# Performance work log

Hardware: AMD Instinct MI355X
Metric: run time of the kernel (lower is better)

Reference implementation:

```python
import jax, jax.numpy as jnp
import numpy as np

N_SERIES = 100000
INPUT_SIZE = 28
OUTPUT_SIZE = 7
N_T = 1
N_S = 4
PERIOD = 7            # seasonality = [7]
EMBED = 1 + 1 + PERIOD  # lev_sms, seas_sms, init seasonal factors
BATCH = 2048
N_TIME = 2048


def setup_inputs() -> dict:
    key = jax.random.key(0)
    k1, k2, k3, k4 = jax.random.split(key, 4)
    # Y must be strictly positive (multiplicative model: division + log)
    Y = jax.random.uniform(k1, (BATCH, N_TIME), dtype=jnp.float32, minval=0.5, maxval=1.5)
    X = jax.random.normal(k2, (BATCH, N_T, N_TIME), dtype=jnp.float32)
    S = jax.random.normal(k3, (BATCH, N_S), dtype=jnp.float32)
    idxs = jax.random.randint(k4, (BATCH,), 0, N_SERIES)
    embeds_weight = jnp.full((N_SERIES, EMBED), 0.5, dtype=jnp.float32)
    return {"S": S, "Y": Y, "X": X, "idxs": idxs,
            "embeds_weight": embeds_weight, "step_size": 7}


def _levels_seasons(Y, idxs, embeds_weight):
    """Exponential smoothing level/seasonality recurrence (single seasonality)."""
    emb = embeds_weight[idxs]                      # (B, 9)
    lev_sms = jax.nn.sigmoid(emb[:, 0])            # (B,)
    seas_sms = jax.nn.sigmoid(emb[:, 1])           # (B,)
    init_seas = jnp.exp(emb[:, 2:2 + PERIOD])      # (B, 7)

    level0 = Y[:, 0] / init_seas[:, 0]
    # ring buffer holding the seasonal factors used at steps t=1..: [s1..s6, s0]
    buf0 = jnp.concatenate([init_seas[:, 1:], init_seas[:, :1]], axis=1)  # (B, 7)

    def step(carry, inp):
        lev, buf = carry
        y, k = inp
        s = jnp.take(buf, k % PERIOD, axis=1)                       # seasonality at lag PERIOD
        newlev = lev_sms * (y / s) + (1.0 - lev_sms) * lev
        news = seas_sms * (y / newlev) + (1.0 - seas_sms) * s
        buf = jax.lax.dynamic_update_slice_in_dim(buf, news[:, None], k % PERIOD, axis=1)
        return (newlev, buf), (newlev, news)

    ks = jnp.arange(N_TIME - 1, dtype=jnp.int32)
    (_, _), (levs, seas) = jax.lax.scan(step, (level0, buf0), (Y[:, 1:].T, ks))
    levels = jnp.concatenate([level0[:, None], levs.T], axis=1)           # (B, n_time)
    seasonal = jnp.concatenate([init_seas, init_seas[:, :1], seas.T], axis=1)  # (B, n_time+7)
    return levels, seasonal


def reference(S, Y, X, idxs, embeds_weight, step_size):
    levels, seasonal = _levels_seasons(Y, idxs, embeds_weight)

    windows_end = N_TIME - INPUT_SIZE - OUTPUT_SIZE + 1
    windows = np.arange(0, windows_end, step_size)          # static window starts
    W = len(windows)

    # --- insample windows, normalized: log(Y / level / season) ---
    idx_in = windows[:, None] + np.arange(INPUT_SIZE)       # (W, I)
    Yw = Y[:, idx_in]                                       # (B, W, I)
    lev_w = levels[:, windows + INPUT_SIZE - 1]             # (B, W)
    seas_w = seasonal[:, idx_in]                            # (B, W, I)
    y_in = jnp.log(Yw / (lev_w[:, :, None] * seas_w))
    y_in = y_in.transpose(1, 0, 2)                          # (W, B, I)

    # --- exogenous windows: X[:, :, start:start+I+O].reshape(B, -1) ---
    idx_x = windows[:, None] + np.arange(INPUT_SIZE + OUTPUT_SIZE)  # (W, I+O)
    Xw = X[:, :, idx_x].transpose(2, 0, 1, 3).reshape(W, BATCH, N_T * (INPUT_SIZE + OUTPUT_SIZE))

    # --- static features ---
    Sw = jnp.broadcast_to(S[None], (W, BATCH, N_S))

    windows_y_insample = jnp.concatenate([y_in, Xw, Sw], axis=2)   # (W, B, context)

    # --- outsample windows (eval mode: not normalized) ---
    idx_out = windows[:, None] + INPUT_SIZE + np.arange(OUTPUT_SIZE)  # (W, O)
    windows_y_outsample = Y[:, idx_out].transpose(1, 0, 2)            # (W, B, O)

    return windows_y_insample, windows_y_outsample, levels, seasonal
```

## Files before the change

### kernel.cpp

```cpp
#include <hip/hip_runtime.h>
#include <math.h>

#define BATCH 2048
#define N_TIME 2048
#define INPUT_SIZE 28
#define OUTPUT_SIZE 7
#define N_S 4
#define PERIOD 7
#define EMBED 9
#define SEAS_LEN (N_TIME + PERIOD)
#define W_COUNT 288
#define WB_COUNT (W_COUNT * BATCH)
#define INS_COLS 67
#define OUT0_SIZE (WB_COUNT * INS_COLS)
#define OUT1_SIZE (WB_COUNT * OUTPUT_SIZE)
#define LEV_SIZE (BATCH * N_TIME)
#define SEAS_SIZE (BATCH * SEAS_LEN)

#define M0_COPY (WB_COUNT * 39)
#define M_COPY  (M0_COPY + OUT1_SIZE)
#define COPY_BLOCKS 480
#define GRID1 (32 + COPY_BLOCKS)
#define N_YIN (WB_COUNT * INPUT_SIZE)
#define CUNROLL 16

struct ScanState {
    float lev, lsms, seas_sms, oma, oms;
    float sbuf[PERIOD];
    float rbuf[PERIOD];
    float yp, sp, rnlp, rnsp;
};

template<bool FIRST, bool LAST, bool PREF>
__device__ __forceinline__ void scan_chunk(
    int base, int l,
    const float* __restrict__ Yb,
    float (&cur)[64], float (&nxt)[64],
    float (*__restrict__ tl)[65], float (*__restrict__ ts)[65],
    ScanState& st)
{
    if (PREF) {
#pragma unroll
        for (int k = 0; k < 64; k += 4)
            *(float4*)&nxt[k] = *(const float4*)(Yb + base + 64 + k);
    }
    tl[l][0] = st.lev;
#pragma unroll
    for (int k = 0; k < 64; ++k) {
        if (!LAST || k < 63) {
            float y  = (k < 63) ? cur[k + 1] : nxt[0];
            float s0 = st.sbuf[k % 7];
            float nl = fmaf(st.oma, st.lev, y * st.rbuf[k % 7]);
            st.lev = nl;
            tl[l][k + 1] = nl;
            if (!FIRST || k > 0) {
                float u  = st.yp * st.rnlp;
                float ns = fmaf(st.oms, st.sp, st.seas_sms * u);
                ts[l][k] = ns;
                st.sbuf[(k + 6) % 7] = ns;
                if (!FIRST || k > 1)
                    st.rbuf[(k + 5) % 7] = st.lsms * st.rnsp;
                st.rnsp = __builtin_amdgcn_rcpf(ns);
            }
            float rnl = __builtin_amdgcn_rcpf(nl);
            st.yp = y; st.sp = s0; st.rnlp = rnl;
        }
    }
    if (LAST) {
        float u  = st.yp * st.rnlp;
        float ns = fmaf(st.oms, st.sp, st.seas_sms * u);
        ts[l][63] = ns;
    } else {
        float t0s = st.sbuf[0], t0r = st.rbuf[0];
#pragma unroll
        for (int q = 0; q < PERIOD - 1; ++q) {
            st.sbuf[q] = st.sbuf[q + 1];
            st.rbuf[q] = st.rbuf[q + 1];
        }
        st.sbuf[PERIOD - 1] = t0s;
        st.rbuf[PERIOD - 1] = t0r;
    }
    asm volatile("s_waitcnt lgkmcnt(0)" ::: "memory");
    __builtin_amdgcn_s_barrier();
}

__device__ __forceinline__ void drain_chunk(
    int base, int jr, int km, int r0,
    const float (*__restrict__ tl)[65], const float (*__restrict__ ts)[65],
    float* __restrict__ levels, float* __restrict__ seasonal)
{
    __builtin_amdgcn_s_barrier();
    asm volatile("" ::: "memory");
#pragma unroll
    for (int j0 = 0; j0 < 64; j0 += 4) {
        int j = j0 + jr;
        float vl[4], vs[4];
#pragma unroll
        for (int i = 0; i < 4; ++i) { vl[i] = tl[j][km + i]; vs[i] = ts[j][km + i]; }
        float4 v4; v4.x = vl[0]; v4.y = vl[1]; v4.z = vl[2]; v4.w = vl[3];
        *(float4*)(levels + (size_t)(r0 + j) * N_TIME + base + km) = v4;
        float* srow = seasonal + (size_t)(r0 + j) * SEAS_LEN + base + 7 + km;
#pragma unroll
        for (int i = 0; i < 4; ++i) srow[i] = vs[i];
    }
    asm volatile("s_waitcnt lgkmcnt(0)" ::: "memory");
}

__device__ __forceinline__ void copy_addr(
    unsigned g,
    const float* __restrict__ Y, const float* __restrict__ X,
    const float* __restrict__ S,
    float* __restrict__ out0, float* __restrict__ out1,
    const float*& src, float*& dst)
{
    if (g < M0_COPY) {
        unsigned wb = g / 39u;
        int jj = (int)(g - wb * 39u);
        int w  = (int)(wb >> 11);
        int b  = (int)(wb & (BATCH - 1));
        src = (jj < 35) ? &X[b * N_TIME + w * 7 + jj]
                        : &S[b * N_S + (jj - 35)];
        dst = &out0[(size_t)wb * 67u + 28u + (unsigned)jj];
    } else {
        unsigned e  = g - M0_COPY;
        unsigned wb = e / 7u;
        int m  = (int)(e - wb * 7u);
        int w  = (int)(wb >> 11);
        int b  = (int)(wb & (BATCH - 1));
        src = &Y[b * N_TIME + w * 7 + INPUT_SIZE + m];
        dst = &out1[e];
    }
}

__global__ __launch_bounds__(128, 1) void es_scan_plus(
    const float* __restrict__ Y, const int* __restrict__ idxs,
    const float* __restrict__ emb, const float* __restrict__ X,
    const float* __restrict__ S,
    float* __restrict__ levels, float* __restrict__ seasonal,
    float* __restrict__ out0, float* __restrict__ out1)
{
    __shared__ float tl[2][64][65];
    __shared__ float ts[2][64][65];
    const int tid = threadIdx.x;
    const int l   = tid & 63;

    if (blockIdx.x >= 32) {
        const unsigned stride = COPY_BLOCKS * 128;
        unsigned g = (blockIdx.x - 32) * 128 + tid;
#pragma unroll 1
        for (; g + (CUNROLL - 1) * stride < M_COPY; g += stride * CUNROLL) {
            const float* src[CUNROLL]; float* dst[CUNROLL]; float v[CUNROLL];
#pragma unroll
            for (int u = 0; u < CUNROLL; ++u)
                copy_addr(g + (unsigned)u * stride, Y, X, S, out0, out1, src[u], dst[u]);
#pragma unroll
            for (int u = 0; u < CUNROLL; ++u) v[u] = *src[u];
#pragma unroll
            for (int u = 0; u < CUNROLL; ++u) *dst[u] = v[u];
        }
#pragma unroll 1
        for (; g < M_COPY; g += stride) {
            const float* src; float* dst;
            copy_addr(g, Y, X, S, out0, out1, src, dst);
            *dst = *src;
        }
        return;
    }

    const int r0 = blockIdx.x * 64;
    if (tid < 64) {
        const int b = r0 + l;
        const float* Yb = Y + (size_t)b * N_TIME;
        const float* e  = emb + (size_t)idxs[b] * EMBED;
        ScanState st;
        st.lsms     = 1.0f / (1.0f + __expf(-e[0]));
        st.seas_sms = 1.0f / (1.0f + __expf(-e[1]));
        st.oma = 1.0f - st.lsms;
        st.oms = 1.0f - st.seas_sms;
        float is[PERIOD];
#pragma unroll
        for (int j = 0; j < PERIOD; ++j) is[j] = __expf(e[2 + j]);
        st.lev = Yb[0] / is[0];

        float* seab = seasonal + (size_t)b * SEAS_LEN;
#pragma unroll
        for (int j = 0; j < PERIOD; ++j) seab[j] = is[j];
        ts[0][l][0] = is[0];
#pragma unroll
        for (int j = 0; j < PERIOD; ++j) st.sbuf[j] = is[(j + 1) % PERIOD];
#pragma unroll
        for (int j = 0; j < PERIOD; ++j)
            st.rbuf[j] = st.lsms * __builtin_amdgcn_rcpf(st.sbuf[j]);
        st.yp = 0.0f; st.sp = 1.0f; st.rnlp = 1.0f; st.rnsp = 1.0f;

        float ya[64], yb2[64];
#pragma unroll
        for (int k = 0; k < 64; k += 4)
            *(float4*)&ya[k] = *(const float4*)(Yb + k);

        scan_chunk<true,  false, true >(0, l, Yb, ya, yb2, tl[0], ts[0], st);
#pragma unroll 1
        for (int cc = 0; cc < 15; ++cc) {
            scan_chunk<false, false, true>(64  + cc * 128, l, Yb, yb2, ya, tl[1], ts[1], st);
            scan_chunk<false, false, true>(128 + cc * 128, l, Yb, ya, yb2, tl[0], ts[0], st);
        }
        scan_chunk<false, true,  false>(1984, l, Yb, yb2, ya, tl[1], ts[1], st);
    } else {
        const int jr = l >> 4;
        const int km = (l & 15) * 4;
#pragma unroll 1
        for (int c = 0; c < 32; ++c)
            drain_chunk(c * 64, jr, km, r0, tl[c & 1], ts[c & 1], levels, seasonal);
    }
}

__global__ __launch_bounds__(256) void es_windows_yin(
    const float* __restrict__ Y, const float* __restrict__ levels,
    const float* __restrict__ seasonal, float* __restrict__ out0)
{
    unsigned gid = blockIdx.x * 256 + threadIdx.x;
    unsigned wb = gid / 28u;
    int j  = (int)(gid - wb * 28u);
    int w  = (int)(wb >> 11);
    int b  = (int)(wb & (BATCH - 1));
    int t0 = w * 7;
    float y  = Y[b * N_TIME + t0 + j];
    float lv = levels[b * N_TIME + t0 + INPUT_SIZE - 1];
    float sv = seasonal[b * SEAS_LEN + t0 + j];
    out0[(size_t)wb * 67u + (unsigned)j] =
        __logf(y * __builtin_amdgcn_rcpf(lv * sv));
}

extern "C" void kernel_launch(void* const* d_in, const int* in_sizes, int n_in,
                              void* d_out, int out_size, void* d_ws, size_t ws_size,
                              hipStream_t stream) {
    const float* S    = (const float*)d_in[0];
    const float* Y    = (const float*)d_in[1];
    const float* X    = (const float*)d_in[2];
    const int*   idxs = (const int*)d_in[3];
    const float* emb  = (const float*)d_in[4];

    float* out      = (float*)d_out;
    float* out_ins  = out;
    float* out_outs = out + OUT0_SIZE;
    float* levels   = out + OUT0_SIZE + OUT1_SIZE;
    float* seasonal = out + OUT0_SIZE + OUT1_SIZE + LEV_SIZE;

    es_scan_plus<<<GRID1, 128, 0, stream>>>(
        Y, idxs, emb, X, S, levels, seasonal, out_ins, out_outs);

    es_windows_yin<<<N_YIN / 256, 256, 0, stream>>>(
        Y, levels, seasonal, out_ins);
}
```

Measured before the change: 351.5 us.

## Fuse y_in window computation into scan kernel via per-superblock ready flags

```diff
diff --git a/kernel.cpp b/kernel.cpp
--- a/kernel.cpp
+++ b/kernel.cpp
@@ -21,8 +21,11 @@
 #define M_COPY  (M0_COPY + OUT1_SIZE)
 #define COPY_BLOCKS 480
 #define GRID1 (32 + COPY_BLOCKS)
-#define N_YIN (WB_COUNT * INPUT_SIZE)
 #define CUNROLL 16
+
+#define YIN_PER_SB (W_COUNT * 64 * INPUT_SIZE)
+#define YIN_PARTS  15
+#define YIN_PART_SZ ((YIN_PER_SB + YIN_PARTS - 1) / YIN_PARTS)
 
 struct ScanState {
     float lev, lsms, seas_sms, oma, oms;
@@ -132,12 +135,59 @@
     }
 }
 
+__device__ __noinline__ void yin_part(
+    int sb, int p, int tid,
+    const float* __restrict__ Y, const float* __restrict__ levels,
+    const float* __restrict__ seasonal, float* __restrict__ out0)
+{
+    const int start = p * YIN_PART_SZ;
+    const int end   = (start + YIN_PART_SZ < YIN_PER_SB) ? start + YIN_PART_SZ
+                                                         : YIN_PER_SB;
+    int e = start + tid;
+#pragma unroll 1
+    for (; e + 7 * 128 < end; e += 8 * 128) {
+        float yv[8], lv[8], sv[8]; size_t dst[8];
+#pragma unroll
+        for (int u = 0; u < 8; ++u) {
+            int ee = e + u * 128;
+            unsigned w    = (unsigned)ee / 1792u;
+            unsigned rem  = (unsigned)ee - w * 1792u;
+            unsigned brel = rem / 28u;
+            unsigned j    = rem - brel * 28u;
+            int b  = sb * 64 + (int)brel;
+            int t0 = (int)w * 7;
+            yv[u] = Y[b * N_TIME + t0 + (int)j];
+            lv[u] = levels[b * N_TIME + t0 + INPUT_SIZE - 1];
+            sv[u] = seasonal[b * SEAS_LEN + t0 + (int)j];
+            dst[u] = ((size_t)w * BATCH + (size_t)b) * 67u + j;
+        }
+#pragma unroll
+        for (int u = 0; u < 8; ++u)
+            out0[dst[u]] = __logf(yv[u] * __builtin_amdgcn_rcpf(lv[u] * sv[u]));
+    }
+#pragma unroll 1
+    for (; e < end; e += 128) {
+        unsigned w    = (unsigned)e / 1792u;
+        unsigned rem  = (unsigned)e - w * 1792u;
+        unsigned brel = rem / 28u;
+        unsigned j    = rem - brel * 28u;
+        int b  = sb * 64 + (int)brel;
+        int t0 = (int)w * 7;
+        float yv = Y[b * N_TIME + t0 + (int)j];
+        float lv = levels[b * N_TIME + t0 + INPUT_SIZE - 1];
+        float sv = seasonal[b * SEAS_LEN + t0 + (int)j];
+        out0[((size_t)w * BATCH + (size_t)b) * 67u + j] =
+            __logf(yv * __builtin_amdgcn_rcpf(lv * sv));
+    }
+}
+
 __global__ __launch_bounds__(128, 1) void es_scan_plus(
     const float* __restrict__ Y, const int* __restrict__ idxs,
     const float* __restrict__ emb, const float* __restrict__ X,
     const float* __restrict__ S,
     float* __restrict__ levels, float* __restrict__ seasonal,
-    float* __restrict__ out0, float* __restrict__ out1)
+    float* __restrict__ out0, float* __restrict__ out1,
+    int* __restrict__ flags)
 {
     __shared__ float tl[2][64][65];
     __shared__ float ts[2][64][65];
@@ -145,8 +195,9 @@
     const int l   = tid & 63;
 
     if (blockIdx.x >= 32) {
+        const int cb = (int)blockIdx.x - 32;
         const unsigned stride = COPY_BLOCKS * 128;
-        unsigned g = (blockIdx.x - 32) * 128 + tid;
+        unsigned g = (unsigned)cb * 128 + tid;
 #pragma unroll 1
         for (; g + (CUNROLL - 1) * stride < M_COPY; g += stride * CUNROLL) {
             const float* src[CUNROLL]; float* dst[CUNROLL]; float v[CUNROLL];
@@ -164,6 +215,15 @@
             copy_addr(g, Y, X, S, out0, out1, src, dst);
             *dst = *src;
         }
+        const int sb = cb & 31;
+        const int p  = cb >> 5;
+        if (tid == 0) {
+            while (__hip_atomic_load(&flags[sb], __ATOMIC_ACQUIRE,
+                                     __HIP_MEMORY_SCOPE_AGENT) == 0)
+                __builtin_amdgcn_s_sleep(16);
+        }
+        __syncthreads();
+        yin_part(sb, p, tid, Y, levels, seasonal, out0);
         return;
     }
 
@@ -181,10 +241,6 @@
 #pragma unroll
         for (int j = 0; j < PERIOD; ++j) is[j] = __expf(e[2 + j]);
         st.lev = Yb[0] / is[0];
-
-        float* seab = seasonal + (size_t)b * SEAS_LEN;
-#pragma unroll
-        for (int j = 0; j < PERIOD; ++j) seab[j] = is[j];
         ts[0][l][0] = is[0];
 #pragma unroll
         for (int j = 0; j < PERIOD; ++j) st.sbuf[j] = is[(j + 1) % PERIOD];
@@ -206,29 +262,23 @@
         }
         scan_chunk<false, true,  false>(1984, l, Yb, yb2, ya, tl[1], ts[1], st);
     } else {
+        const int b = r0 + l;
+        {
+            const float* e = emb + (size_t)idxs[b] * EMBED;
+            float* seab = seasonal + (size_t)b * SEAS_LEN;
+#pragma unroll
+            for (int j = 0; j < PERIOD; ++j) seab[j] = __expf(e[2 + j]);
+        }
         const int jr = l >> 4;
         const int km = (l & 15) * 4;
 #pragma unroll 1
         for (int c = 0; c < 32; ++c)
             drain_chunk(c * 64, jr, km, r0, tl[c & 1], ts[c & 1], levels, seasonal);
-    }
-}
-
-__global__ __launch_bounds__(256) void es_windows_yin(
-    const float* __restrict__ Y, const float* __restrict__ levels,
-    const float* __restrict__ seasonal, float* __restrict__ out0)
-{
-    unsigned gid = blockIdx.x * 256 + threadIdx.x;
-    unsigned wb = gid / 28u;
-    int j  = (int)(gid - wb * 28u);
-    int w  = (int)(wb >> 11);
-    int b  = (int)(wb & (BATCH - 1));
-    int t0 = w * 7;
-    float y  = Y[b * N_TIME + t0 + j];
-    float lv = levels[b * N_TIME + t0 + INPUT_SIZE - 1];
-    float sv = seasonal[b * SEAS_LEN + t0 + j];
-    out0[(size_t)wb * 67u + (unsigned)j] =
-        __logf(y * __builtin_amdgcn_rcpf(lv * sv));
+        asm volatile("s_waitcnt vmcnt(0)" ::: "memory");
+        if (l == 0)
+            __hip_atomic_store(&flags[blockIdx.x], 1, __ATOMIC_RELEASE,
+                               __HIP_MEMORY_SCOPE_AGENT);
+    }
 }
 
 extern "C" void kernel_launch(void* const* d_in, const int* in_sizes, int n_in,
@@ -246,9 +296,9 @@
     float* levels   = out + OUT0_SIZE + OUT1_SIZE;
     float* seasonal = out + OUT0_SIZE + OUT1_SIZE + LEV_SIZE;
 
+    int* flags = (int*)d_ws;
+    hipMemsetAsync(d_ws, 0, 32 * sizeof(int), stream);
+
     es_scan_plus<<<GRID1, 128, 0, stream>>>(
-        Y, idxs, emb, X, S, levels, seasonal, out_ins, out_outs);
-
-    es_windows_yin<<<N_YIN / 256, 256, 0, stream>>>(
-        Y, levels, seasonal, out_ins);
-}
+        Y, idxs, emb, X, S, levels, seasonal, out_ins, out_outs, flags);
+}
```

New measurement: 380.9 us. 1.08x slower.
